# Kernel optimization log

Hardware: AMD Instinct MI355X
Metric: run time of the kernel (lower is better)

Reference implementation:

```python
import jax, jax.numpy as jnp
import numpy as np

B, C, D = 1024, 100, 768


def setup_inputs() -> dict:
    key = jax.random.key(0)
    k1, k2, k3, k4 = jax.random.split(key, 4)
    raw_features = jax.random.normal(k1, (B, D), dtype=jnp.float32)
    class_means = jax.random.normal(k2, (C, D), dtype=jnp.float32)
    # stand-in for per-class pinv of shrunk+normalized covariance
    class_inv_covs = jax.random.normal(k3, (C, D, D), dtype=jnp.float32) * 0.02
    # diag_std is positive (clamped at 1e-6 in the original)
    class_diags = jax.random.uniform(k4, (C, D), dtype=jnp.float32, minval=0.5, maxval=1.5)
    return {
        "raw_features": raw_features,
        "class_means": class_means,
        "class_inv_covs": class_inv_covs,
        "class_diags": class_diags,
    }


def reference(raw_features, class_means, class_inv_covs, class_diags):
    # Batched over classes: diff[b,c,d] = raw[b,d]/diag[c,d] - mean[c,d]/diag[c,d]
    diff = (raw_features[:, None, :] - class_means[None, :, :]) / class_diags[None, :, :]  # [B,C,D]
    # temp[b,c,e] = sum_d diff[b,c,d] * inv[c,d,e]  (the per-class diff @ inv_c)
    temp = jnp.einsum('bcd,cde->bce', diff, class_inv_covs)
    dist_sq = jnp.sum(temp * diff, axis=-1)  # [B,C]
    return -dist_sq  # scores_stack
```

## Files before the change

kernel.cpp:

```cpp
#include <hip/hip_runtime.h>
#include <hip/hip_bf16.h>

#define B_SZ 1024
#define C_SZ 100
#define D_SZ 768

#define BM 128
#define BN 128
#define BK 64
#define NKT (D_SZ / BK)
#define NTHREADS 256
#define TPC 48

#define A_BUF (BM * BK)
#define X_BUF (BN * BK)

#define TBL_ELEMS ((size_t)C_SZ * D_SZ)
#define AP_ELEMS  ((size_t)C_SZ * D_SZ * D_SZ)
#define RB_ELEMS  ((size_t)B_SZ * D_SZ)

typedef float f32x4 __attribute__((ext_vector_type(4)));
typedef short short8 __attribute__((ext_vector_type(8)));

__device__ __forceinline__ ushort f2bf(float f) {
    union { __hip_bfloat16 b; ushort u; } cv; cv.b = __float2bfloat16(f); return cv.u;
}
__device__ __forceinline__ float bf2f(ushort u) {
    union { __hip_bfloat16 b; ushort us; } cv; cv.us = u; return __bfloat162float(cv.b);
}
__device__ __forceinline__ void gload_lds16(const void* g, void* l) {
    __builtin_amdgcn_global_load_lds((const __attribute__((address_space(1))) void*)g,
                                     (__attribute__((address_space(3))) void*)l, 16, 0, 0);
}

__global__ __launch_bounds__(256) void make_tables(const float* __restrict__ mean,
                                                   const float* __restrict__ diag,
                                                   float* __restrict__ rd,
                                                   float* __restrict__ md) {
    const int i = ((int)blockIdx.x * 256 + (int)threadIdx.x) * 4;
    if (i < (int)TBL_ELEMS) {
        const f32x4 dv = *(const f32x4*)(diag + i);
        const f32x4 mv = *(const f32x4*)(mean + i);
        f32x4 r, m;
        r.x = 1.0f / dv.x; r.y = 1.0f / dv.y; r.z = 1.0f / dv.z; r.w = 1.0f / dv.w;
        m.x = mv.x * r.x;  m.y = mv.y * r.y;  m.z = mv.z * r.z;  m.w = mv.w * r.w;
        *(f32x4*)(rd + i) = r;
        *(f32x4*)(md + i) = m;
    }
}

__global__ __launch_bounds__(256) void conv_rawbf(const float* __restrict__ raw,
                                                  ushort* __restrict__ rb) {
    const size_t i = (size_t)blockIdx.x * 256 + threadIdx.x;
    const f32x4 v0 = *(const f32x4*)(raw + i * 8);
    const f32x4 v1 = *(const f32x4*)(raw + i * 8 + 4);
    short8 p;
    p[0]=(short)f2bf(v0.x); p[1]=(short)f2bf(v0.y); p[2]=(short)f2bf(v0.z); p[3]=(short)f2bf(v0.w);
    p[4]=(short)f2bf(v1.x); p[5]=(short)f2bf(v1.y); p[6]=(short)f2bf(v1.z); p[7]=(short)f2bf(v1.w);
    *(short8*)(rb + i * 8) = p;
}

__global__ __launch_bounds__(512) void conv_aprime(const float* __restrict__ inv,
                                                   const float* __restrict__ rd,
                                                   const float* __restrict__ md,
                                                   ushort* __restrict__ ap,
                                                   float* __restrict__ w) {
    const int lane = (int)threadIdx.x & 63;
    const int wv   = (int)threadIdx.x >> 6;
    const int ridx = (int)blockIdx.x * 8 + wv;
    const int c    = ridx / D_SZ;
    const float* arow = inv + (size_t)ridx * D_SZ;
    const float* rdc  = rd + (size_t)c * D_SZ;
    const float* mdc  = md + (size_t)c * D_SZ;
    ushort* aprow = ap + (size_t)ridx * D_SZ;
    float dot = 0.f;
    #pragma unroll
    for (int j = 0; j < 3; ++j) {
        const int e = j * 256 + lane * 4;
        const f32x4 a  = *(const f32x4*)(arow + e);
        const f32x4 r4 = *(const f32x4*)(rdc + e);
        const f32x4 m4 = *(const f32x4*)(mdc + e);
        dot += a.x * m4.x + a.y * m4.y + a.z * m4.z + a.w * m4.w;
        ushort4 p;
        p.x = f2bf(a.x * r4.x); p.y = f2bf(a.y * r4.y);
        p.z = f2bf(a.z * r4.z); p.w = f2bf(a.w * r4.w);
        *(ushort4*)(aprow + e) = p;
    }
    #pragma unroll
    for (int k = 1; k < 64; k <<= 1) dot += __shfl_xor(dot, k);
    if (lane == 0) w[ridx] = dot;
}

template <int MODE>
__global__ __launch_bounds__(NTHREADS, 2) void fecam_scores(
        const float* __restrict__ raw, const float* __restrict__ mean,
        const float* __restrict__ diag, const float* __restrict__ inv,
        const float* __restrict__ rdT, const float* __restrict__ mdT,
        const float* __restrict__ wT,
        const ushort* __restrict__ apAll, const ushort* __restrict__ rbAll,
        float* __restrict__ out) {
    __shared__ __align__(16) ushort aLds[2 * A_BUF];
    __shared__ __align__(16) ushort xLds[2 * X_BUF];
    __shared__ float red[4 * 64];

    const int tid = (int)threadIdx.x;
    const int bx  = (int)blockIdx.x;

    const int x = bx & 7;
    const int slot0 = bx >> 3;
    const int nCls  = (x < 4) ? 13 : 12;
    const int baseC = (x < 4) ? x * 13 : 52 + (x - 4) * 12;
    const int ci = slot0 / TPC;
    if (ci >= nCls) return;
    const int t  = slot0 % TPC;
    const int c  = baseC + ci;
    const int d0 = (t >> 3) * BM;
    const int b0 = (t & 7) * BN;

    const int lane = tid & 63;
    const int wid  = tid >> 6;
    const int wm   = wid >> 1;
    const int wn   = wid & 1;
    const int l15  = lane & 15;
    const int l4   = lane >> 4;

    const ushort* apc = apAll + (size_t)c * D_SZ * D_SZ;
    const float*  Af  = inv + (size_t)c * D_SZ * D_SZ;

    auto stage = [&](int buf, int kt) {
        #pragma unroll
        for (int i = 0; i < 4; ++i) {
            const int s = tid + i * NTHREADS;
            const int r = s >> 3;
            const int q = (s & 7) ^ (r & 7);
            if constexpr (MODE == 2) {
                gload_lds16(apc + (size_t)(d0 + r) * D_SZ + kt * BK + q * 8,
                            aLds + buf * A_BUF + s * 8);
            } else {
                const float* gp = Af + (size_t)(d0 + r) * D_SZ + kt * BK + q * 8;
                const f32x4 a0 = *(const f32x4*)gp;
                const f32x4 a1 = *(const f32x4*)(gp + 4);
                short8 p;
                p[0]=(short)f2bf(a0.x); p[1]=(short)f2bf(a0.y); p[2]=(short)f2bf(a0.z); p[3]=(short)f2bf(a0.w);
                p[4]=(short)f2bf(a1.x); p[5]=(short)f2bf(a1.y); p[6]=(short)f2bf(a1.z); p[7]=(short)f2bf(a1.w);
                *(short8*)(aLds + buf * A_BUF + s * 8) = p;
            }
        }
        #pragma unroll
        for (int i = 0; i < 4; ++i) {
            const int s = tid + i * NTHREADS;
            const int r = s >> 3;
            const int q = (s & 7) ^ (r & 7);
            const int e = kt * BK + q * 8;
            if constexpr (MODE == 2) {
                gload_lds16(rbAll + (size_t)(b0 + r) * D_SZ + e,
                            xLds + buf * X_BUF + s * 8);
            } else {
                const float* rp = raw + (size_t)(b0 + r) * D_SZ + e;
                const f32x4 r0 = *(const f32x4*)rp, r1 = *(const f32x4*)(rp + 4);
                const f32x4 mm0 = *(const f32x4*)(mean + (size_t)c * D_SZ + e);
                const f32x4 mm1 = *(const f32x4*)(mean + (size_t)c * D_SZ + e + 4);
                const f32x4 gg0 = *(const f32x4*)(diag + (size_t)c * D_SZ + e);
                const f32x4 gg1 = *(const f32x4*)(diag + (size_t)c * D_SZ + e + 4);
                short8 p;
                p[0]=(short)f2bf((r0.x-mm0.x)/gg0.x); p[1]=(short)f2bf((r0.y-mm0.y)/gg0.y);
                p[2]=(short)f2bf((r0.z-mm0.z)/gg0.z); p[3]=(short)f2bf((r0.w-mm0.w)/gg0.w);
                p[4]=(short)f2bf((r1.x-mm1.x)/gg1.x); p[5]=(short)f2bf((r1.y-mm1.y)/gg1.y);
                p[6]=(short)f2bf((r1.z-mm1.z)/gg1.z); p[7]=(short)f2bf((r1.w-mm1.w)/gg1.w);
                *(short8*)(xLds + buf * X_BUF + s * 8) = p;
            }
        }
    };

    f32x4 acc[4][4] = {};

    auto compute = [&](int buf) {
        const ushort* ab = aLds + buf * A_BUF;
        const ushort* xb = xLds + buf * X_BUF;
        #pragma unroll
        for (int kk = 0; kk < 2; ++kk) {
            const int fc = (kk * 4 + l4) ^ (l15 & 7);
            short8 xf[4];
            #pragma unroll
            for (int n = 0; n < 4; ++n)
                xf[n] = *(const short8*)(xb + (wn * 64 + n * 16 + l15) * 64 + fc * 8);
            __builtin_amdgcn_s_setprio(1);
            #pragma unroll
            for (int m = 0; m < 4; ++m) {
                const short8 af = *(const short8*)(ab + (wm * 64 + m * 16 + l15) * 64 + fc * 8);
                #pragma unroll
                for (int n = 0; n < 4; ++n)
                    acc[m][n] = __builtin_amdgcn_mfma_f32_16x16x32_bf16(af, xf[n], acc[m][n], 0, 0, 0);
            }
            __builtin_amdgcn_s_setprio(0);
        }
    };

    stage(0, 0);
    __syncthreads();
    for (int kt = 0; kt < NKT; ++kt) {
        const int cur = kt & 1;
        if (kt + 1 < NKT) stage(cur ^ 1, kt + 1);
        compute(cur);
        __syncthreads();
    }

    float v[4] = {};
    #pragma unroll
    for (int m = 0; m < 4; ++m) {
        const int dd = d0 + wm * 64 + m * 16 + l4 * 4;
        f32x4 rd4, md4, w4;
        if constexpr (MODE == 2) {
            rd4 = *(const f32x4*)(rdT + (size_t)c * D_SZ + dd);
            md4 = *(const f32x4*)(mdT + (size_t)c * D_SZ + dd);
            w4  = *(const f32x4*)(wT + (size_t)c * D_SZ + dd);
        } else {
            const f32x4 mm4 = *(const f32x4*)(mean + (size_t)c * D_SZ + dd);
            const f32x4 gg4 = *(const f32x4*)(diag + (size_t)c * D_SZ + dd);
            rd4.x = 1.0f/gg4.x; rd4.y = 1.0f/gg4.y; rd4.z = 1.0f/gg4.z; rd4.w = 1.0f/gg4.w;
            md4.x = mm4.x*rd4.x; md4.y = mm4.y*rd4.y; md4.z = mm4.z*rd4.z; md4.w = mm4.w*rd4.w;
            w4.x = 0.f; w4.y = 0.f; w4.z = 0.f; w4.w = 0.f;
        }
        #pragma unroll
        for (int n = 0; n < 4; ++n) {
            const int bl = b0 + wn * 64 + n * 16 + l15;
            const f32x4 rv = *(const f32x4*)(raw + (size_t)bl * D_SZ + dd);
            v[n] += (w4.x - acc[m][n][0]) * (rv.x * rd4.x - md4.x)
                  + (w4.y - acc[m][n][1]) * (rv.y * rd4.y - md4.y)
                  + (w4.z - acc[m][n][2]) * (rv.z * rd4.z - md4.z)
                  + (w4.w - acc[m][n][3]) * (rv.w * rd4.w - md4.w);
        }
    }
    #pragma unroll
    for (int n = 0; n < 4; ++n) {
        v[n] += __shfl_xor(v[n], 16);
        v[n] += __shfl_xor(v[n], 32);
    }
    if (lane < 16) {
        #pragma unroll
        for (int n = 0; n < 4; ++n) red[wid * 64 + n * 16 + l15] = v[n];
    }
    __syncthreads();
    if (tid < BN) {
        const int wnn = tid >> 6;
        const int off = tid & 63;
        const float p = red[wnn * 64 + off] + red[(wnn + 2) * 64 + off];
        atomicAdd(out + (size_t)(b0 + tid) * C_SZ + c, p);
    }
}

extern "C" void kernel_launch(void* const* d_in, const int* in_sizes, int n_in,
                              void* d_out, int out_size, void* d_ws, size_t ws_size,
                              hipStream_t stream) {
    const float* raw  = (const float*)d_in[0];
    const float* mean = (const float*)d_in[1];
    const float* inv  = (const float*)d_in[2];
    const float* diag = (const float*)d_in[3];
    float* out = (float*)d_out;

    const size_t TBL_B = TBL_ELEMS * 4;
    const size_t AP_B  = AP_ELEMS * 2;
    const size_t RB_B  = RB_ELEMS * 2;
    const size_t need  = 3 * TBL_B + AP_B + RB_B;

    hipMemsetAsync(d_out, 0, (size_t)out_size * sizeof(float), stream);
    dim3 grid(8 * 13 * TPC);

    if (ws_size >= need) {
        float*  rdT = (float*)d_ws;
        float*  mdT = (float*)((char*)d_ws + TBL_B);
        float*  wT  = (float*)((char*)d_ws + 2 * TBL_B);
        ushort* ap  = (ushort*)((char*)d_ws + 3 * TBL_B);
        ushort* rb  = (ushort*)((char*)d_ws + 3 * TBL_B + AP_B);
        make_tables<<<75, 256, 0, stream>>>(mean, diag, rdT, mdT);
        conv_rawbf<<<384, 256, 0, stream>>>(raw, rb);
        conv_aprime<<<9600, 512, 0, stream>>>(inv, rdT, mdT, ap, wT);
        fecam_scores<2><<<grid, NTHREADS, 0, stream>>>(raw, mean, diag, inv,
                                                       rdT, mdT, wT, ap, rb, out);
    } else {
        fecam_scores<0><<<grid, NTHREADS, 0, stream>>>(raw, mean, diag, inv,
                                                       nullptr, nullptr, nullptr,
                                                       nullptr, nullptr, out);
    }
}
```

Measured before the change: 247.0 us.

## Process four batch tiles per block in a persistent loop over N

Each block now walks four consecutive 128-row batch tiles for its class and D slice, instead of one tile per block. The grid shrinks from 4992 to 1248 blocks, and staging of the next batch tile's first K slice overlaps the current tile's last compute step. The epilogue folds accumulators per tile and issues atomics per wave directly, removing the shared-memory reduction and its extra barrier, which doubles the atomic count. The A operand still reloads for every batch tile, so the gain comes mainly from fewer launches or blocks and a continuous pipeline, at the cost of less parallelism.

```diff
diff --git a/kernel.cpp b/kernel.cpp
--- a/kernel.cpp
+++ b/kernel.cpp
@@ -10,7 +10,7 @@
 #define BK 64
 #define NKT (D_SZ / BK)
 #define NTHREADS 256
-#define TPC 48
+#define NTILES 4
 
 #define A_BUF (BM * BK)
 #define X_BUF (BN * BK)
@@ -101,7 +101,6 @@
         float* __restrict__ out) {
     __shared__ __align__(16) ushort aLds[2 * A_BUF];
     __shared__ __align__(16) ushort xLds[2 * X_BUF];
-    __shared__ float red[4 * 64];
 
     const int tid = (int)threadIdx.x;
     const int bx  = (int)blockIdx.x;
@@ -110,12 +109,12 @@
     const int slot0 = bx >> 3;
     const int nCls  = (x < 4) ? 13 : 12;
     const int baseC = (x < 4) ? x * 13 : 52 + (x - 4) * 12;
-    const int ci = slot0 / TPC;
+    const int ci = slot0 / 12;
     if (ci >= nCls) return;
-    const int t  = slot0 % TPC;
-    const int c  = baseC + ci;
-    const int d0 = (t >> 3) * BM;
-    const int b0 = (t & 7) * BN;
+    const int sub = slot0 % 12;
+    const int c   = baseC + ci;
+    const int d0  = (sub >> 1) * BM;
+    const int bh0 = (sub & 1) * (NTILES * BN);
 
     const int lane = tid & 63;
     const int wid  = tid >> 6;
@@ -127,7 +126,7 @@
     const ushort* apc = apAll + (size_t)c * D_SZ * D_SZ;
     const float*  Af  = inv + (size_t)c * D_SZ * D_SZ;
 
-    auto stage = [&](int buf, int kt) {
+    auto stage = [&](int buf, int b0n, int kt) {
         #pragma unroll
         for (int i = 0; i < 4; ++i) {
             const int s = tid + i * NTHREADS;
@@ -153,10 +152,10 @@
             const int q = (s & 7) ^ (r & 7);
             const int e = kt * BK + q * 8;
             if constexpr (MODE == 2) {
-                gload_lds16(rbAll + (size_t)(b0 + r) * D_SZ + e,
+                gload_lds16(rbAll + (size_t)(b0n + r) * D_SZ + e,
                             xLds + buf * X_BUF + s * 8);
             } else {
-                const float* rp = raw + (size_t)(b0 + r) * D_SZ + e;
+                const float* rp = raw + (size_t)(b0n + r) * D_SZ + e;
                 const f32x4 r0 = *(const f32x4*)rp, r1 = *(const f32x4*)(rp + 4);
                 const f32x4 mm0 = *(const f32x4*)(mean + (size_t)c * D_SZ + e);
                 const f32x4 mm1 = *(const f32x4*)(mean + (size_t)c * D_SZ + e + 4);
@@ -196,56 +195,64 @@
         }
     };
 
-    stage(0, 0);
+    auto fold = [&](int b0n) {
+        float v[4] = {};
+        #pragma unroll
+        for (int m = 0; m < 4; ++m) {
+            const int dd = d0 + wm * 64 + m * 16 + l4 * 4;
+            f32x4 rd4, md4, w4;
+            if constexpr (MODE == 2) {
+                rd4 = *(const f32x4*)(rdT + (size_t)c * D_SZ + dd);
+                md4 = *(const f32x4*)(mdT + (size_t)c * D_SZ + dd);
+                w4  = *(const f32x4*)(wT + (size_t)c * D_SZ + dd);
+            } else {
+                const f32x4 mm4 = *(const f32x4*)(mean + (size_t)c * D_SZ + dd);
+                const f32x4 gg4 = *(const f32x4*)(diag + (size_t)c * D_SZ + dd);
+                rd4.x = 1.0f/gg4.x; rd4.y = 1.0f/gg4.y; rd4.z = 1.0f/gg4.z; rd4.w = 1.0f/gg4.w;
+                md4.x = mm4.x*rd4.x; md4.y = mm4.y*rd4.y; md4.z = mm4.z*rd4.z; md4.w = mm4.w*rd4.w;
+                w4.x = 0.f; w4.y = 0.f; w4.z = 0.f; w4.w = 0.f;
+            }
+            #pragma unroll
+            for (int n = 0; n < 4; ++n) {
+                const int bl = b0n + wn * 64 + n * 16 + l15;
+                const f32x4 rv = *(const f32x4*)(raw + (size_t)bl * D_SZ + dd);
+                v[n] += (w4.x - acc[m][n][0]) * (rv.x * rd4.x - md4.x)
+                      + (w4.y - acc[m][n][1]) * (rv.y * rd4.y - md4.y)
+                      + (w4.z - acc[m][n][2]) * (rv.z * rd4.z - md4.z)
+                      + (w4.w - acc[m][n][3]) * (rv.w * rd4.w - md4.w);
+                acc[m][n] = (f32x4){0.f, 0.f, 0.f, 0.f};
+            }
+        }
+        #pragma unroll
+        for (int n = 0; n < 4; ++n) {
+            v[n] += __shfl_xor(v[n], 16);
+            v[n] += __shfl_xor(v[n], 32);
+        }
+        if (lane < 16) {
+            #pragma unroll
+            for (int n = 0; n < 4; ++n)
+                atomicAdd(out + (size_t)(b0n + wn * 64 + n * 16 + l15) * C_SZ + c, v[n]);
+        }
+    };
+
+    stage(0, bh0, 0);
     __syncthreads();
-    for (int kt = 0; kt < NKT; ++kt) {
-        const int cur = kt & 1;
-        if (kt + 1 < NKT) stage(cur ^ 1, kt + 1);
-        compute(cur);
-        __syncthreads();
-    }
-
-    float v[4] = {};
-    #pragma unroll
-    for (int m = 0; m < 4; ++m) {
-        const int dd = d0 + wm * 64 + m * 16 + l4 * 4;
-        f32x4 rd4, md4, w4;
-        if constexpr (MODE == 2) {
-            rd4 = *(const f32x4*)(rdT + (size_t)c * D_SZ + dd);
-            md4 = *(const f32x4*)(mdT + (size_t)c * D_SZ + dd);
-            w4  = *(const f32x4*)(wT + (size_t)c * D_SZ + dd);
-        } else {
-            const f32x4 mm4 = *(const f32x4*)(mean + (size_t)c * D_SZ + dd);
-            const f32x4 gg4 = *(const f32x4*)(diag + (size_t)c * D_SZ + dd);
-            rd4.x = 1.0f/gg4.x; rd4.y = 1.0f/gg4.y; rd4.z = 1.0f/gg4.z; rd4.w = 1.0f/gg4.w;
-            md4.x = mm4.x*rd4.x; md4.y = mm4.y*rd4.y; md4.z = mm4.z*rd4.z; md4.w = mm4.w*rd4.w;
-            w4.x = 0.f; w4.y = 0.f; w4.z = 0.f; w4.w = 0.f;
-        }
-        #pragma unroll
-        for (int n = 0; n < 4; ++n) {
-            const int bl = b0 + wn * 64 + n * 16 + l15;
-            const f32x4 rv = *(const f32x4*)(raw + (size_t)bl * D_SZ + dd);
-            v[n] += (w4.x - acc[m][n][0]) * (rv.x * rd4.x - md4.x)
-                  + (w4.y - acc[m][n][1]) * (rv.y * rd4.y - md4.y)
-                  + (w4.z - acc[m][n][2]) * (rv.z * rd4.z - md4.z)
-                  + (w4.w - acc[m][n][3]) * (rv.w * rd4.w - md4.w);
-        }
-    }
-    #pragma unroll
-    for (int n = 0; n < 4; ++n) {
-        v[n] += __shfl_xor(v[n], 16);
-        v[n] += __shfl_xor(v[n], 32);
-    }
-    if (lane < 16) {
-        #pragma unroll
-        for (int n = 0; n < 4; ++n) red[wid * 64 + n * 16 + l15] = v[n];
-    }
-    __syncthreads();
-    if (tid < BN) {
-        const int wnn = tid >> 6;
-        const int off = tid & 63;
-        const float p = red[wnn * 64 + off] + red[(wnn + 2) * 64 + off];
-        atomicAdd(out + (size_t)(b0 + tid) * C_SZ + c, p);
+
+    int cur = 0;
+    for (int nt = 0; nt < NTILES; ++nt) {
+        const int b0n = bh0 + nt * BN;
+        for (int kt = 0; kt < NKT; ++kt) {
+            const bool last = (nt == NTILES - 1) && (kt == NKT - 1);
+            if (!last) {
+                int nkt = kt + 1, nb = b0n;
+                if (nkt == NKT) { nkt = 0; nb = b0n + BN; }
+                stage(cur ^ 1, nb, nkt);
+            }
+            compute(cur);
+            __syncthreads();
+            cur ^= 1;
+        }
+        fold(b0n);
     }
 }
 
@@ -264,7 +271,7 @@
     const size_t need  = 3 * TBL_B + AP_B + RB_B;
 
     hipMemsetAsync(d_out, 0, (size_t)out_size * sizeof(float), stream);
-    dim3 grid(8 * 13 * TPC);
+    dim3 grid(8 * 13 * 12);
 
     if (ws_size >= need) {
         float*  rdT = (float*)d_ws;
```

Result: slower. 406.7 us (+64.6%).

## Deepen MODE 2 load pipeline to four LDS slots with BK 32

Applied to the files above, without the earlier changes.

Halves the K tile to 32 and allocates four LDS slots, so the MODE 2 path keeps three direct-to-LDS global loads in flight. It waits with explicit s_waitcnt vmcnt counts plus a raw barrier instead of a full __syncthreads per iteration. The swizzle is reworked for the 4-chunk rows. This is meant to hide global memory latency better, at the cost of twice as many iterations and barriers, and the correctness depends on the hand-counted vmcnt values.

```diff
diff --git a/kernel.cpp b/kernel.cpp
--- a/kernel.cpp
+++ b/kernel.cpp
@@ -7,10 +7,11 @@
 
 #define BM 128
 #define BN 128
-#define BK 64
+#define BK 32
 #define NKT (D_SZ / BK)
 #define NTHREADS 256
 #define TPC 48
+#define NSLOT 4
 
 #define A_BUF (BM * BK)
 #define X_BUF (BN * BK)
@@ -99,8 +100,8 @@
         const float* __restrict__ wT,
         const ushort* __restrict__ apAll, const ushort* __restrict__ rbAll,
         float* __restrict__ out) {
-    __shared__ __align__(16) ushort aLds[2 * A_BUF];
-    __shared__ __align__(16) ushort xLds[2 * X_BUF];
+    __shared__ __align__(16) ushort aLds[NSLOT * A_BUF];
+    __shared__ __align__(16) ushort xLds[NSLOT * X_BUF];
     __shared__ float red[4 * 64];
 
     const int tid = (int)threadIdx.x;
@@ -127,15 +128,15 @@
     const ushort* apc = apAll + (size_t)c * D_SZ * D_SZ;
     const float*  Af  = inv + (size_t)c * D_SZ * D_SZ;
 
-    auto stage = [&](int buf, int kt) {
-        #pragma unroll
-        for (int i = 0; i < 4; ++i) {
+    auto stage = [&](int slot, int kt) {
+        #pragma unroll
+        for (int i = 0; i < 2; ++i) {
             const int s = tid + i * NTHREADS;
-            const int r = s >> 3;
-            const int q = (s & 7) ^ (r & 7);
+            const int r = s >> 2;
+            const int q = (s & 3) ^ ((r >> 1) & 3);
             if constexpr (MODE == 2) {
                 gload_lds16(apc + (size_t)(d0 + r) * D_SZ + kt * BK + q * 8,
-                            aLds + buf * A_BUF + s * 8);
+                            aLds + slot * A_BUF + s * 8);
             } else {
                 const float* gp = Af + (size_t)(d0 + r) * D_SZ + kt * BK + q * 8;
                 const f32x4 a0 = *(const f32x4*)gp;
@@ -143,18 +144,18 @@
                 short8 p;
                 p[0]=(short)f2bf(a0.x); p[1]=(short)f2bf(a0.y); p[2]=(short)f2bf(a0.z); p[3]=(short)f2bf(a0.w);
                 p[4]=(short)f2bf(a1.x); p[5]=(short)f2bf(a1.y); p[6]=(short)f2bf(a1.z); p[7]=(short)f2bf(a1.w);
-                *(short8*)(aLds + buf * A_BUF + s * 8) = p;
+                *(short8*)(aLds + slot * A_BUF + s * 8) = p;
             }
         }
         #pragma unroll
-        for (int i = 0; i < 4; ++i) {
+        for (int i = 0; i < 2; ++i) {
             const int s = tid + i * NTHREADS;
-            const int r = s >> 3;
-            const int q = (s & 7) ^ (r & 7);
+            const int r = s >> 2;
+            const int q = (s & 3) ^ ((r >> 1) & 3);
             const int e = kt * BK + q * 8;
             if constexpr (MODE == 2) {
                 gload_lds16(rbAll + (size_t)(b0 + r) * D_SZ + e,
-                            xLds + buf * X_BUF + s * 8);
+                            xLds + slot * X_BUF + s * 8);
             } else {
                 const float* rp = raw + (size_t)(b0 + r) * D_SZ + e;
                 const f32x4 r0 = *(const f32x4*)rp, r1 = *(const f32x4*)(rp + 4);
@@ -167,42 +168,51 @@
                 p[2]=(short)f2bf((r0.z-mm0.z)/gg0.z); p[3]=(short)f2bf((r0.w-mm0.w)/gg0.w);
                 p[4]=(short)f2bf((r1.x-mm1.x)/gg1.x); p[5]=(short)f2bf((r1.y-mm1.y)/gg1.y);
                 p[6]=(short)f2bf((r1.z-mm1.z)/gg1.z); p[7]=(short)f2bf((r1.w-mm1.w)/gg1.w);
-                *(short8*)(xLds + buf * X_BUF + s * 8) = p;
+                *(short8*)(xLds + slot * X_BUF + s * 8) = p;
             }
         }
     };
 
     f32x4 acc[4][4] = {};
 
-    auto compute = [&](int buf) {
-        const ushort* ab = aLds + buf * A_BUF;
-        const ushort* xb = xLds + buf * X_BUF;
-        #pragma unroll
-        for (int kk = 0; kk < 2; ++kk) {
-            const int fc = (kk * 4 + l4) ^ (l15 & 7);
-            short8 xf[4];
+    const int fc = l4 ^ ((l15 >> 1) & 3);
+    auto compute = [&](int slot) {
+        const ushort* ab = aLds + slot * A_BUF;
+        const ushort* xb = xLds + slot * X_BUF;
+        short8 xf[4];
+        #pragma unroll
+        for (int n = 0; n < 4; ++n)
+            xf[n] = *(const short8*)(xb + ((wn * 64 + n * 16 + l15) * 4 + fc) * 8);
+        __builtin_amdgcn_s_setprio(1);
+        #pragma unroll
+        for (int m = 0; m < 4; ++m) {
+            const short8 af = *(const short8*)(ab + ((wm * 64 + m * 16 + l15) * 4 + fc) * 8);
             #pragma unroll
             for (int n = 0; n < 4; ++n)
-                xf[n] = *(const short8*)(xb + (wn * 64 + n * 16 + l15) * 64 + fc * 8);
-            __builtin_amdgcn_s_setprio(1);
-            #pragma unroll
-            for (int m = 0; m < 4; ++m) {
-                const short8 af = *(const short8*)(ab + (wm * 64 + m * 16 + l15) * 64 + fc * 8);
-                #pragma unroll
-                for (int n = 0; n < 4; ++n)
-                    acc[m][n] = __builtin_amdgcn_mfma_f32_16x16x32_bf16(af, xf[n], acc[m][n], 0, 0, 0);
-            }
-            __builtin_amdgcn_s_setprio(0);
-        }
+                acc[m][n] = __builtin_amdgcn_mfma_f32_16x16x32_bf16(af, xf[n], acc[m][n], 0, 0, 0);
+        }
+        __builtin_amdgcn_s_setprio(0);
     };
 
-    stage(0, 0);
-    __syncthreads();
-    for (int kt = 0; kt < NKT; ++kt) {
-        const int cur = kt & 1;
-        if (kt + 1 < NKT) stage(cur ^ 1, kt + 1);
-        compute(cur);
+    if constexpr (MODE == 2) {
+        stage(0, 0); stage(1, 1); stage(2, 2);
+        for (int kt = 0; kt < NKT; ++kt) {
+            if (kt < NKT - 2)       asm volatile("s_waitcnt vmcnt(8)" ::: "memory");
+            else if (kt == NKT - 2) asm volatile("s_waitcnt vmcnt(4)" ::: "memory");
+            else                    asm volatile("s_waitcnt vmcnt(0)" ::: "memory");
+            __builtin_amdgcn_s_barrier();
+            if (kt + 3 < NKT) stage((kt + 3) & 3, kt + 3);
+            compute(kt & 3);
+        }
+    } else {
+        stage(0, 0);
         __syncthreads();
+        for (int kt = 0; kt < NKT; ++kt) {
+            const int cur = kt & 1;
+            if (kt + 1 < NKT) stage(cur ^ 1, kt + 1);
+            compute(cur);
+            __syncthreads();
+        }
     }
 
     float v[4] = {};
```

After: 288.4 us. +16.8%, slower.
